# Kernel tuning notes

Hardware: AMD Instinct MI355X
Metric: run time of the kernel (lower is better)

## Reference

```python
import jax, jax.numpy as jnp
import numpy as np

EMBED_DIM = 512
NUM_HEADS = 8
HEAD_DIM = EMBED_DIM // NUM_HEADS
LN_EPS = 1e-5


def setup_inputs() -> dict:
    key = jax.random.key(0)
    ks = jax.random.split(key, 7)
    B, S, E = 2, 4096, EMBED_DIM
    s = 1.0 / np.sqrt(E)
    return {
        "x": jax.random.normal(ks[0], (B, S, E), dtype=jnp.float32),
        "qkv_w": jax.random.normal(ks[1], (E, 3 * E), dtype=jnp.float32) * s,
        "qkv_b": jax.random.normal(ks[2], (3 * E,), dtype=jnp.float32) * 0.01,
        "out_w": jax.random.normal(ks[3], (E, E), dtype=jnp.float32) * s,
        "out_b": jax.random.normal(ks[4], (E,), dtype=jnp.float32) * 0.01,
        "ln_g": jnp.ones((E,), dtype=jnp.float32),
        "ln_b": jnp.zeros((E,), dtype=jnp.float32),
    }


def reference(x, qkv_w, qkv_b, out_w, out_b, ln_g, ln_b):
    B, S, E = x.shape
    H, D = NUM_HEADS, HEAD_DIM
    scale = D ** -0.5
    qkv = x @ qkv_w + qkv_b                     # (B, S, 3E)
    qkv = qkv.reshape(B, S, 3, H, D)
    q, k, v = qkv[:, :, 0], qkv[:, :, 1], qkv[:, :, 2]  # (B, S, H, D)
    scores = jnp.einsum("bshd,bthd->bhst", q, k) * scale  # (B, H, S, S)
    probs = jax.nn.softmax(scores, axis=-1)
    ctx = jnp.einsum("bhst,bthd->bshd", probs, v).reshape(B, S, E)
    out = ctx @ out_w + out_b + x               # residual
    mu = out.mean(-1, keepdims=True)
    var = out.var(-1, keepdims=True)
    return (out - mu) * jax.lax.rsqrt(var + LN_EPS) * ln_g + ln_b
```

## Files before the change

kernel.cpp:

```cpp
#include <hip/hip_runtime.h>
#include <stdint.h>

typedef __bf16 bf16x8 __attribute__((ext_vector_type(8)));
typedef float f32x4 __attribute__((ext_vector_type(4)));
typedef float f32x16 __attribute__((ext_vector_type(16)));
typedef float float4v __attribute__((ext_vector_type(4)));
typedef unsigned short u16x4 __attribute__((ext_vector_type(4)));
typedef unsigned short u16x8 __attribute__((ext_vector_type(8)));
typedef unsigned int u32x4v __attribute__((ext_vector_type(4)));

#define DEVI __device__ __forceinline__

static constexpr int Bv = 2, Sv = 4096, Ev = 512, Hv = 8, Dv = 64;
static constexpr int Mv = Bv * Sv;
static constexpr int N3v = 3 * Ev;
static constexpr float QSCALE = 0.125f * 1.4426950408889634f;
static constexpr float C0 = -8.0f;

#if __has_builtin(__builtin_amdgcn_exp2f)
#define EXP2F(x) __builtin_amdgcn_exp2f(x)
#else
#define EXP2F(x) exp2f(x)
#endif

DEVI unsigned short f2bf(float f) {
    unsigned int u = __builtin_bit_cast(unsigned int, f);
    u += 0x7fffu + ((u >> 16) & 1u);
    return (unsigned short)(u >> 16);
}

DEVI unsigned int cvtpk(float lo, float hi) {
    unsigned int r;
    asm("v_cvt_pk_bf16_f32 %0, %1, %2" : "=v"(r) : "v"(lo), "v"(hi));
    return r;
}

DEVI void gload16(const void* src, void* lds) {
    __builtin_amdgcn_global_load_lds(
        (const __attribute__((address_space(1))) unsigned int*)src,
        (__attribute__((address_space(3))) unsigned int*)lds,
        16, 0, 0);
}

__global__ __launch_bounds__(256) void k_convert(const float* __restrict__ in,
                                                 unsigned short* __restrict__ out, int n4) {
    int i = blockIdx.x * 256 + threadIdx.x;
    int stride = gridDim.x * 256;
    for (; i < n4; i += stride) {
        float4v v = ((const float4v*)in)[i];
        u16x4 o;
        o[0] = f2bf(v[0]); o[1] = f2bf(v[1]); o[2] = f2bf(v[2]); o[3] = f2bf(v[3]);
        ((u16x4*)out)[i] = o;
    }
}

__global__ __launch_bounds__(256) void k_tconv(const float* __restrict__ in,
                                               unsigned short* __restrict__ out, int K, int N) {
    __shared__ float lds[32][36];
    int tilesN = N >> 5;
    int tn = blockIdx.x % tilesN, tk = blockIdx.x / tilesN;
    int k0 = tk << 5, n0 = tn << 5;
    int t = threadIdx.x;
    int r = t >> 3, c4 = (t & 7) << 2;
    float4v v = *(const float4v*)(in + (size_t)(k0 + r) * N + n0 + c4);
    *(float4v*)&lds[r][c4] = v;
    __syncthreads();
    int nn = t >> 3, kc = (t & 7) << 2;
    u16x4 o;
#pragma unroll
    for (int j = 0; j < 4; ++j) o[j] = f2bf(lds[kc + j][nn]);
    *(u16x4*)(out + (size_t)(n0 + nn) * K + k0 + kc) = o;
}

template <int EPI>
__global__ __launch_bounds__(256) void k_gemm(
    const unsigned short* __restrict__ A, const unsigned short* __restrict__ Bt,
    int M, int N, int K, const float* __restrict__ bias,
    unsigned short* __restrict__ Qb, unsigned short* __restrict__ Kb,
    unsigned short* __restrict__ Vb,
    const float* __restrict__ xres, float* __restrict__ outf) {
    __shared__ char smem[32768];
    char* As = smem;
    char* Bs = smem + 16384;
    int nbt = N >> 7;
    int mb = blockIdx.x / nbt, nbi = blockIdx.x % nbt;
    int m0 = mb << 7, n0 = nbi << 7;
    int tid = threadIdx.x, lane = tid & 63, wave = tid >> 6;
    int wr = wave >> 1, wc = wave & 1;

    f32x4 acc[4][4];
    f32x4 zero = {0.f, 0.f, 0.f, 0.f};
#pragma unroll
    for (int a = 0; a < 4; ++a)
#pragma unroll
        for (int b = 0; b < 4; ++b) acc[a][b] = zero;

    for (int kt = 0; kt < K; kt += 64) {
        __syncthreads();
#pragma unroll
        for (int j = 0; j < 4; ++j) {
            int la = (((wave << 2) + j) << 10) + lane * 16;
            int r = la >> 7, cb = la & 127;
            int cbs = cb ^ ((r & 7) << 4);
            gload16((const char*)(A + (size_t)(m0 + r) * K + kt) + cbs,
                    As + (((wave << 2) + j) << 10));
            gload16((const char*)(Bt + (size_t)(n0 + r) * K + kt) + cbs,
                    Bs + (((wave << 2) + j) << 10));
        }
        asm volatile("s_waitcnt vmcnt(0)" ::: "memory");
        __syncthreads();

        bf16x8 af[4][2], bfr[4][2];
#pragma unroll
        for (int rf = 0; rf < 4; ++rf)
#pragma unroll
            for (int c = 0; c < 2; ++c) {
                int row = (wr << 6) + (rf << 4) + (lane & 15);
                int col = (c << 6) + ((lane >> 4) << 4);
                af[rf][c] = *(const bf16x8*)(As + row * 128 + (col ^ ((row & 7) << 4)));
                int rowb = (wc << 6) + (rf << 4) + (lane & 15);
                bfr[rf][c] = *(const bf16x8*)(Bs + rowb * 128 + (col ^ ((rowb & 7) << 4)));
            }
#pragma unroll
        for (int rf = 0; rf < 4; ++rf)
#pragma unroll
            for (int nf = 0; nf < 4; ++nf)
#pragma unroll
                for (int c = 0; c < 2; ++c)
                    acc[rf][nf] = __builtin_amdgcn_mfma_f32_16x16x32_bf16(
                        af[rf][c], bfr[nf][c], acc[rf][nf], 0, 0, 0);
    }

#pragma unroll
    for (int rf = 0; rf < 4; ++rf)
#pragma unroll
        for (int nf = 0; nf < 4; ++nf)
#pragma unroll
            for (int i = 0; i < 4; ++i) {
                int row = m0 + (wr << 6) + (rf << 4) + ((lane >> 4) << 2) + i;
                int col = n0 + (wc << 6) + (nf << 4) + (lane & 15);
                float v = acc[rf][nf][i] + bias[col];
                if (EPI == 0) {
                    int reg = col >> 9, hd = col & 511;
                    int h = hd >> 6, d = hd & 63;
                    int b = row >> 12, s = row & 4095;
                    size_t idx = ((size_t)((b << 3) + h) * Sv + s) * Dv + d;
                    if (reg == 0)      Qb[idx] = f2bf(v * QSCALE);
                    else if (reg == 1) Kb[idx] = f2bf(v);
                    else               Vb[idx] = f2bf(v);
                } else {
                    v += xres[(size_t)row * N + col];
                    outf[(size_t)row * N + col] = v;
                }
            }
}

__global__ __launch_bounds__(256) void k_transpose_v(const unsigned short* __restrict__ V,
                                                     unsigned short* __restrict__ Vt) {
    __shared__ char lds[8192];
    int bh = blockIdx.x >> 6, st = blockIdx.x & 63;
    int s0 = st << 6;
    int t = threadIdx.x;
#pragma unroll
    for (int j = 0; j < 2; ++j) {
        int r = (t >> 3) + (j << 5);
        int cb = (t & 7) << 4;
        u16x8 v = *(const u16x8*)(V + ((size_t)bh * Sv + s0 + r) * Dv + (cb >> 1));
        *(u16x8*)(lds + r * 128 + (cb ^ ((r & 7) << 4))) = v;
    }
    __syncthreads();
#pragma unroll
    for (int j = 0; j < 2; ++j) {
        int d = (t >> 3) + (j << 5);
        int ss = (t & 7) << 3;
        u16x8 o;
#pragma unroll
        for (int k = 0; k < 8; ++k) {
            int s = ss + k;
            o[k] = *(const unsigned short*)(lds + s * 128 + ((d * 2) ^ ((s & 7) << 4)));
        }
        *(u16x8*)(Vt + ((size_t)bh * Dv + d) * Sv + s0 + ss) = o;
    }
}

__global__ __launch_bounds__(256) void k_attn(const unsigned short* __restrict__ Qb,
                                              const unsigned short* __restrict__ Kb,
                                              const unsigned short* __restrict__ Vtb,
                                              unsigned short* __restrict__ ctx) {
    __shared__ char smem[32768];
    int bid = blockIdx.x;
    int wg = ((bid & 7) << 6) + (bid >> 3);
    int bh = wg >> 5, qblk = wg & 31;
    int b = bh >> 3, h = bh & 7;
    int tid = threadIdx.x, lane = tid & 63, wave = tid >> 6;
    int l31 = lane & 31, hh = lane >> 5;
    int qrow = (qblk << 7) + (wave << 5) + l31;

    const unsigned short* Kbase = Kb + (size_t)bh * Sv * Dv;
    const unsigned short* Vtbase = Vtb + (size_t)bh * Dv * Sv;

    bf16x8 qf[4];
#pragma unroll
    for (int tp = 0; tp < 4; ++tp)
        qf[tp] = *(const bf16x8*)(Qb + ((size_t)bh * Sv + qrow) * Dv + (tp << 4) + (hh << 3));

    const char* src[4];
    int strd[4];
    int ldsoff[4];
#pragma unroll
    for (int j = 0; j < 4; ++j) {
        int off = ((wave << 2) + j) << 10;
        int loff = off + lane * 16;
        ldsoff[j] = off;
        if (off < 8192) {
            int r = loff >> 7, cb = loff & 127;
            src[j] = (const char*)(Kbase + (size_t)r * Dv) + (cb ^ ((r & 7) << 4));
            strd[j] = 64 * Dv * 2;
        } else {
            int lo2 = loff - 8192;
            int r = lo2 >> 7, cb = lo2 & 127;
            src[j] = (const char*)(Vtbase + (size_t)r * Sv) + (cb ^ ((r & 7) << 4));
            strd[j] = 64 * 2;
        }
    }

    int koff[2][4], voff[2][2][2];
#pragma unroll
    for (int c = 0; c < 2; ++c) {
        int krow = (c << 5) + l31;
        int ksw = (krow & 7) << 4;
#pragma unroll
        for (int tp = 0; tp < 4; ++tp)
            koff[c][tp] = krow * 128 + (((tp << 5) + (hh << 4)) ^ ksw);
#pragma unroll
        for (int tl = 0; tl < 2; ++tl) {
            int vcb = (c << 6) + (tl << 5) + (hh << 4);
#pragma unroll
            for (int dt = 0; dt < 2; ++dt) {
                int vrow = (dt << 5) + l31;
                voff[c][tl][dt] = vrow * 128 + (vcb ^ ((vrow & 7) << 4));
            }
        }
    }

    f32x16 o[2];
#pragma unroll
    for (int dt = 0; dt < 2; ++dt)
#pragma unroll
        for (int r = 0; r < 16; ++r) o[dt][r] = 0.f;
    float lsum = 0.f;

#pragma unroll
    for (int j = 0; j < 4; ++j) gload16(src[j], smem + ldsoff[j]);
    __syncthreads();

    for (int kt = 0; kt < 64; ++kt) {
        if (kt < 63) {
            int nb = (kt + 1) & 1;
#pragma unroll
            for (int j = 0; j < 4; ++j)
                gload16(src[j] + (size_t)(kt + 1) * strd[j], smem + nb * 16384 + ldsoff[j]);
        }
        char* Ks = smem + (kt & 1) * 16384;
        char* Vs = Ks + 8192;

#pragma unroll
        for (int c = 0; c < 2; ++c) {
            bf16x8 kf[4];
#pragma unroll
            for (int tp = 0; tp < 4; ++tp)
                kf[tp] = *(const bf16x8*)(Ks + koff[c][tp]);
            f32x16 sc;
#pragma unroll
            for (int r = 0; r < 16; ++r) sc[r] = C0;
#pragma unroll
            for (int tp = 0; tp < 4; ++tp)
                sc = __builtin_amdgcn_mfma_f32_32x32x16_bf16(kf[tp], qf[tp], sc, 0, 0, 0);

            float p[16];
#pragma unroll
            for (int r = 0; r < 16; ++r) p[r] = EXP2F(sc[r]);
            float s0 = (p[0] + p[1]) + (p[2] + p[3]);
            float s1 = (p[4] + p[5]) + (p[6] + p[7]);
            float s2 = (p[8] + p[9]) + (p[10] + p[11]);
            float s3 = (p[12] + p[13]) + (p[14] + p[15]);
            lsum += (s0 + s1) + (s2 + s3);

            unsigned int W[8];
#pragma unroll
            for (int i = 0; i < 8; ++i) W[i] = cvtpk(p[2 * i], p[2 * i + 1]);

#pragma unroll
            for (int tl = 0; tl < 2; ++tl) {
                unsigned int a1 = W[4 * tl], b1 = W[4 * tl + 2];
                unsigned int a2 = W[4 * tl + 1], b2 = W[4 * tl + 3];
                asm volatile("v_permlane32_swap_b32 %0, %1" : "+v"(a1), "+v"(b1));
                asm volatile("v_permlane32_swap_b32 %0, %1" : "+v"(a2), "+v"(b2));
                u32x4v uu;
                uu[0] = a1; uu[1] = a2; uu[2] = b1; uu[3] = b2;
                bf16x8 pf = __builtin_bit_cast(bf16x8, uu);
#pragma unroll
                for (int dt = 0; dt < 2; ++dt) {
                    bf16x8 vf = *(const bf16x8*)(Vs + voff[c][tl][dt]);
                    o[dt] = __builtin_amdgcn_mfma_f32_32x32x16_bf16(vf, pf, o[dt], 0, 0, 0);
                }
            }
        }
        __syncthreads();
    }

    lsum += __shfl_xor(lsum, 32, 64);
    float inv = 1.f / lsum;
    size_t obase = ((size_t)b * Sv + qrow) * Ev + (h << 6);
#pragma unroll
    for (int dt = 0; dt < 2; ++dt)
#pragma unroll
        for (int rp = 0; rp < 8; ++rp) {
            int r = rp << 1;
            int d = (dt << 5) + (r & 3) + ((r >> 2) << 3) + (hh << 2);
            unsigned int w = cvtpk(o[dt][r] * inv, o[dt][r + 1] * inv);
            *(unsigned int*)(ctx + obase + d) = w;
        }
}

__global__ __launch_bounds__(256) void k_ln(const float* __restrict__ in,
                                            const float* __restrict__ g,
                                            const float* __restrict__ bta,
                                            float* __restrict__ out) {
    int wave = threadIdx.x >> 6, lane = threadIdx.x & 63;
    size_t row = (size_t)blockIdx.x * 4 + wave;
    const float* p = in + row * 512 + lane * 8;
    float4v v0 = *(const float4v*)p;
    float4v v1 = *(const float4v*)(p + 4);
    float s = 0.f, q = 0.f;
#pragma unroll
    for (int j = 0; j < 4; ++j) {
        s += v0[j] + v1[j];
        q += v0[j] * v0[j] + v1[j] * v1[j];
    }
#pragma unroll
    for (int off = 1; off < 64; off <<= 1) {
        s += __shfl_xor(s, off, 64);
        q += __shfl_xor(q, off, 64);
    }
    float mu = s * (1.f / 512.f);
    float var = q * (1.f / 512.f) - mu * mu;
    float rs = rsqrtf(var + 1e-5f);
    int c = lane * 8;
    float4v o0, o1;
#pragma unroll
    for (int j = 0; j < 4; ++j) {
        o0[j] = (v0[j] - mu) * rs * g[c + j] + bta[c + j];
        o1[j] = (v1[j] - mu) * rs * g[c + 4 + j] + bta[c + 4 + j];
    }
    *(float4v*)(out + row * 512 + c) = o0;
    *(float4v*)(out + row * 512 + c + 4) = o1;
}

extern "C" void kernel_launch(void* const* d_in, const int* in_sizes, int n_in,
                              void* d_out, int out_size, void* d_ws, size_t ws_size,
                              hipStream_t stream) {
    const float* x     = (const float*)d_in[0];
    const float* qkv_w = (const float*)d_in[1];
    const float* qkv_b = (const float*)d_in[2];
    const float* out_w = (const float*)d_in[3];
    const float* out_b = (const float*)d_in[4];
    const float* ln_g  = (const float*)d_in[5];
    const float* ln_b  = (const float*)d_in[6];
    float* out = (float*)d_out;
    char* ws = (char*)d_ws;

    unsigned short* xb    = (unsigned short*)(ws);
    unsigned short* wqkvT = (unsigned short*)(ws + 8388608);
    unsigned short* owT   = (unsigned short*)(ws + 9961472);
    unsigned short* Qb    = (unsigned short*)(ws + 10485760);
    unsigned short* Kb    = (unsigned short*)(ws + 18874368);
    unsigned short* Vb    = (unsigned short*)(ws + 27262976);
    unsigned short* Vtb   = (unsigned short*)(ws + 35651584);
    unsigned short* ctxb  = (unsigned short*)(ws + 44040192);
    float* tmp            = (float*)(ws + 52428800);

    k_convert<<<2048, 256, 0, stream>>>(x, xb, Mv * Ev / 4);
    k_tconv<<<(512 / 32) * (1536 / 32), 256, 0, stream>>>(qkv_w, wqkvT, 512, 1536);
    k_tconv<<<(512 / 32) * (512 / 32), 256, 0, stream>>>(out_w, owT, 512, 512);
    k_gemm<0><<<(Mv / 128) * (N3v / 128), 256, 0, stream>>>(
        xb, wqkvT, Mv, N3v, Ev, qkv_b, Qb, Kb, Vb, nullptr, nullptr);
    k_transpose_v<<<16 * 64, 256, 0, stream>>>(Vb, Vtb);
    k_attn<<<512, 256, 0, stream>>>(Qb, Kb, Vtb, ctxb);
    k_gemm<1><<<(Mv / 128) * (Ev / 128), 256, 0, stream>>>(
        ctxb, owT, Mv, Ev, Ev, out_b, nullptr, nullptr, nullptr, x, tmp);
    k_ln<<<Mv / 4, 256, 0, stream>>>(tmp, ln_g, ln_b, out);
}
```

Baseline: 164.8 us.

## Split attention KV range across two blocks, merge partials, fuse V transpose

Attention is split along the key/value sequence into two halves, so twice as many workgroups run. Each half writes unnormalized bf16 partial outputs and row sums, and a new merge kernel adds the two halves and normalizes. This works because softmax uses a fixed offset rather than a running max. The QKV GEMM epilogue now writes V directly in transposed layout, which removes the separate transpose kernel, and s_setprio is raised around the MFMA sections. The cost is an extra kernel, extra partial-output traffic, and bf16 rounding of the unnormalized partials.

```diff
diff --git a/kernel.cpp b/kernel.cpp
--- a/kernel.cpp
+++ b/kernel.cpp
@@ -27,6 +27,10 @@
     unsigned int u = __builtin_bit_cast(unsigned int, f);
     u += 0x7fffu + ((u >> 16) & 1u);
     return (unsigned short)(u >> 16);
+}
+
+DEVI float b2f(unsigned short u) {
+    return __builtin_bit_cast(float, (unsigned int)u << 16);
 }
 
 DEVI unsigned int cvtpk(float lo, float hi) {
@@ -77,7 +81,7 @@
     const unsigned short* __restrict__ A, const unsigned short* __restrict__ Bt,
     int M, int N, int K, const float* __restrict__ bias,
     unsigned short* __restrict__ Qb, unsigned short* __restrict__ Kb,
-    unsigned short* __restrict__ Vb,
+    unsigned short* __restrict__ Vtb,
     const float* __restrict__ xres, float* __restrict__ outf) {
     __shared__ char smem[32768];
     char* As = smem;
@@ -134,70 +138,55 @@
 #pragma unroll
     for (int rf = 0; rf < 4; ++rf)
 #pragma unroll
-        for (int nf = 0; nf < 4; ++nf)
-#pragma unroll
-            for (int i = 0; i < 4; ++i) {
-                int row = m0 + (wr << 6) + (rf << 4) + ((lane >> 4) << 2) + i;
-                int col = n0 + (wc << 6) + (nf << 4) + (lane & 15);
-                float v = acc[rf][nf][i] + bias[col];
-                if (EPI == 0) {
-                    int reg = col >> 9, hd = col & 511;
-                    int h = hd >> 6, d = hd & 63;
-                    int b = row >> 12, s = row & 4095;
-                    size_t idx = ((size_t)((b << 3) + h) * Sv + s) * Dv + d;
-                    if (reg == 0)      Qb[idx] = f2bf(v * QSCALE);
-                    else if (reg == 1) Kb[idx] = f2bf(v);
-                    else               Vb[idx] = f2bf(v);
+        for (int nf = 0; nf < 4; ++nf) {
+            int row0 = m0 + (wr << 6) + (rf << 4) + ((lane >> 4) << 2);
+            int col = n0 + (wc << 6) + (nf << 4) + (lane & 15);
+            float bv = bias[col];
+            if (EPI == 0) {
+                int reg = col >> 9, hd = col & 511;
+                int h = hd >> 6, d = hd & 63;
+                int b = row0 >> 12, s0 = row0 & 4095;
+                if (reg == 2) {
+                    u16x4 o4;
+#pragma unroll
+                    for (int i = 0; i < 4; ++i) o4[i] = f2bf(acc[rf][nf][i] + bv);
+                    *(u16x4*)(Vtb + ((size_t)((b << 3) + h) * 64 + d) * 4096 + s0) = o4;
                 } else {
-                    v += xres[(size_t)row * N + col];
+#pragma unroll
+                    for (int i = 0; i < 4; ++i) {
+                        float v = acc[rf][nf][i] + bv;
+                        size_t idx = ((size_t)((b << 3) + h) * Sv + s0 + i) * Dv + d;
+                        if (reg == 0) Qb[idx] = f2bf(v * QSCALE);
+                        else          Kb[idx] = f2bf(v);
+                    }
+                }
+            } else {
+#pragma unroll
+                for (int i = 0; i < 4; ++i) {
+                    int row = row0 + i;
+                    float v = acc[rf][nf][i] + bv + xres[(size_t)row * N + col];
                     outf[(size_t)row * N + col] = v;
                 }
             }
-}
-
-__global__ __launch_bounds__(256) void k_transpose_v(const unsigned short* __restrict__ V,
-                                                     unsigned short* __restrict__ Vt) {
-    __shared__ char lds[8192];
-    int bh = blockIdx.x >> 6, st = blockIdx.x & 63;
-    int s0 = st << 6;
-    int t = threadIdx.x;
-#pragma unroll
-    for (int j = 0; j < 2; ++j) {
-        int r = (t >> 3) + (j << 5);
-        int cb = (t & 7) << 4;
-        u16x8 v = *(const u16x8*)(V + ((size_t)bh * Sv + s0 + r) * Dv + (cb >> 1));
-        *(u16x8*)(lds + r * 128 + (cb ^ ((r & 7) << 4))) = v;
-    }
-    __syncthreads();
-#pragma unroll
-    for (int j = 0; j < 2; ++j) {
-        int d = (t >> 3) + (j << 5);
-        int ss = (t & 7) << 3;
-        u16x8 o;
-#pragma unroll
-        for (int k = 0; k < 8; ++k) {
-            int s = ss + k;
-            o[k] = *(const unsigned short*)(lds + s * 128 + ((d * 2) ^ ((s & 7) << 4)));
-        }
-        *(u16x8*)(Vt + ((size_t)bh * Dv + d) * Sv + s0 + ss) = o;
-    }
+        }
 }
 
 __global__ __launch_bounds__(256) void k_attn(const unsigned short* __restrict__ Qb,
                                               const unsigned short* __restrict__ Kb,
                                               const unsigned short* __restrict__ Vtb,
-                                              unsigned short* __restrict__ ctx) {
+                                              unsigned short* __restrict__ po,
+                                              float* __restrict__ pl) {
     __shared__ char smem[32768];
     int bid = blockIdx.x;
-    int wg = ((bid & 7) << 6) + (bid >> 3);
-    int bh = wg >> 5, qblk = wg & 31;
-    int b = bh >> 3, h = bh & 7;
+    int wg = ((bid & 7) << 7) + (bid >> 3);
+    int half = wg & 1, qblk = (wg >> 1) & 31, bh = wg >> 6;
     int tid = threadIdx.x, lane = tid & 63, wave = tid >> 6;
     int l31 = lane & 31, hh = lane >> 5;
     int qrow = (qblk << 7) + (wave << 5) + l31;
-
-    const unsigned short* Kbase = Kb + (size_t)bh * Sv * Dv;
-    const unsigned short* Vtbase = Vtb + (size_t)bh * Dv * Sv;
+    int kvbase = half << 11;
+
+    const unsigned short* Kbase = Kb + (size_t)bh * Sv * Dv + (size_t)kvbase * Dv;
+    const unsigned short* Vtbase = Vtb + (size_t)bh * Dv * Sv + kvbase;
 
     bf16x8 qf[4];
 #pragma unroll
@@ -254,8 +243,8 @@
     for (int j = 0; j < 4; ++j) gload16(src[j], smem + ldsoff[j]);
     __syncthreads();
 
-    for (int kt = 0; kt < 64; ++kt) {
-        if (kt < 63) {
+    for (int kt = 0; kt < 32; ++kt) {
+        if (kt < 31) {
             int nb = (kt + 1) & 1;
 #pragma unroll
             for (int j = 0; j < 4; ++j)
@@ -273,9 +262,11 @@
             f32x16 sc;
 #pragma unroll
             for (int r = 0; r < 16; ++r) sc[r] = C0;
+            __builtin_amdgcn_s_setprio(1);
 #pragma unroll
             for (int tp = 0; tp < 4; ++tp)
                 sc = __builtin_amdgcn_mfma_f32_32x32x16_bf16(kf[tp], qf[tp], sc, 0, 0, 0);
+            __builtin_amdgcn_s_setprio(0);
 
             float p[16];
 #pragma unroll
@@ -299,28 +290,51 @@
                 u32x4v uu;
                 uu[0] = a1; uu[1] = a2; uu[2] = b1; uu[3] = b2;
                 bf16x8 pf = __builtin_bit_cast(bf16x8, uu);
+                __builtin_amdgcn_s_setprio(1);
 #pragma unroll
                 for (int dt = 0; dt < 2; ++dt) {
                     bf16x8 vf = *(const bf16x8*)(Vs + voff[c][tl][dt]);
                     o[dt] = __builtin_amdgcn_mfma_f32_32x32x16_bf16(vf, pf, o[dt], 0, 0, 0);
                 }
+                __builtin_amdgcn_s_setprio(0);
             }
         }
         __syncthreads();
     }
 
     lsum += __shfl_xor(lsum, 32, 64);
-    float inv = 1.f / lsum;
-    size_t obase = ((size_t)b * Sv + qrow) * Ev + (h << 6);
+    if (!hh) pl[((size_t)half * 16 + bh) * Sv + qrow] = lsum;
+    size_t obase = (((size_t)half * 16 + bh) * Sv + qrow) * 64;
 #pragma unroll
     for (int dt = 0; dt < 2; ++dt)
 #pragma unroll
         for (int rp = 0; rp < 8; ++rp) {
             int r = rp << 1;
             int d = (dt << 5) + (r & 3) + ((r >> 2) << 3) + (hh << 2);
-            unsigned int w = cvtpk(o[dt][r] * inv, o[dt][r + 1] * inv);
-            *(unsigned int*)(ctx + obase + d) = w;
-        }
+            unsigned int w = cvtpk(o[dt][r], o[dt][r + 1]);
+            *(unsigned int*)(po + obase + d) = w;
+        }
+}
+
+__global__ __launch_bounds__(256) void k_merge(const unsigned short* __restrict__ po,
+                                               const float* __restrict__ pl,
+                                               unsigned short* __restrict__ ctx) {
+    int t = blockIdx.x * 256 + threadIdx.x;
+    int d8 = t & 7, s = (t >> 3) & 4095, bh = t >> 15;
+    int b = bh >> 3, h = bh & 7;
+    size_t r0 = ((size_t)bh * 4096 + s) * 64 + (d8 << 3);
+    size_t r1 = r0 + (size_t)16 * 4096 * 64;
+    u16x8 pa = *(const u16x8*)(po + r0);
+    u16x8 pb = *(const u16x8*)(po + r1);
+    float inv = 1.f / (pl[(size_t)bh * 4096 + s] + pl[(size_t)16 * 4096 + bh * 4096 + s]);
+    u32x4v w;
+#pragma unroll
+    for (int j = 0; j < 4; ++j) {
+        float lo = (b2f(pa[2 * j]) + b2f(pb[2 * j])) * inv;
+        float hi = (b2f(pa[2 * j + 1]) + b2f(pb[2 * j + 1])) * inv;
+        w[j] = cvtpk(lo, hi);
+    }
+    *(u32x4v*)(ctx + ((size_t)b * 4096 + s) * 512 + (h << 6) + (d8 << 3)) = w;
 }
 
 __global__ __launch_bounds__(256) void k_ln(const float* __restrict__ in,
@@ -375,18 +389,19 @@
     unsigned short* owT   = (unsigned short*)(ws + 9961472);
     unsigned short* Qb    = (unsigned short*)(ws + 10485760);
     unsigned short* Kb    = (unsigned short*)(ws + 18874368);
-    unsigned short* Vb    = (unsigned short*)(ws + 27262976);
-    unsigned short* Vtb   = (unsigned short*)(ws + 35651584);
-    unsigned short* ctxb  = (unsigned short*)(ws + 44040192);
-    float* tmp            = (float*)(ws + 52428800);
+    unsigned short* Vtb   = (unsigned short*)(ws + 27262976);
+    unsigned short* ctxb  = (unsigned short*)(ws + 35651584);
+    unsigned short* po    = (unsigned short*)(ws + 44040192);
+    float* tmp            = (float*)(ws + 44040192);
+    float* pl             = (float*)(ws + 60817408);
 
     k_convert<<<2048, 256, 0, stream>>>(x, xb, Mv * Ev / 4);
     k_tconv<<<(512 / 32) * (1536 / 32), 256, 0, stream>>>(qkv_w, wqkvT, 512, 1536);
     k_tconv<<<(512 / 32) * (512 / 32), 256, 0, stream>>>(out_w, owT, 512, 512);
     k_gemm<0><<<(Mv / 128) * (N3v / 128), 256, 0, stream>>>(
-        xb, wqkvT, Mv, N3v, Ev, qkv_b, Qb, Kb, Vb, nullptr, nullptr);
-    k_transpose_v<<<16 * 64, 256, 0, stream>>>(Vb, Vtb);
-    k_attn<<<512, 256, 0, stream>>>(Qb, Kb, Vtb, ctxb);
+        xb, wqkvT, Mv, N3v, Ev, qkv_b, Qb, Kb, Vtb, nullptr, nullptr);
+    k_attn<<<1024, 256, 0, stream>>>(Qb, Kb, Vtb, po, pl);
+    k_merge<<<2048, 256, 0, stream>>>(po, pl, ctxb);
     k_gemm<1><<<(Mv / 128) * (Ev / 128), 256, 0, stream>>>(
         ctxb, owT, Mv, Ev, Ev, out_b, nullptr, nullptr, nullptr, x, tmp);
     k_ln<<<Mv / 4, 256, 0, stream>>>(tmp, ln_g, ln_b, out);
```

Result: faster. 160.8 us (-2.4%).
